# Kernel tuning notes

Hardware: AMD Instinct MI355X
Metric: run time of the kernel (lower is better)

Reference implementation:

```python
import math
import jax, jax.numpy as jnp
import numpy as np

H = 1024
N = 64
DT_MIN, DT_MAX = 0.001, 0.1
L_CONST = 4096


def setup_inputs() -> dict:
    key = jax.random.key(0)
    k1, k2 = jax.random.split(key)
    log_dt = jax.random.uniform(k1, (H,), dtype=jnp.float32) * (
        math.log(DT_MAX) - math.log(DT_MIN)
    ) + math.log(DT_MIN)
    C = jax.random.normal(k2, (H, N // 2, 2), dtype=jnp.float32)  # real view of complex C
    log_A_real = jnp.log(0.5 * jnp.ones((H, N // 2), dtype=jnp.float32))
    A_imag = math.pi * jnp.tile(jnp.arange(N // 2, dtype=jnp.float32)[None, :], (H, 1))
    return {"L": L_CONST, "log_dt": log_dt, "C": C, "log_A_real": log_A_real, "A_imag": A_imag}


def reference(L, log_dt, C, log_A_real, A_imag):
    dt = jnp.exp(log_dt)                                  # (H,)
    Cc = C[..., 0] + 1j * C[..., 1]                        # (H, N/2) complex
    A = -jnp.exp(log_A_real) + 1j * A_imag                 # (H, N/2) complex
    dtA = A * dt[:, None]                                  # (H, N/2)
    t = jnp.arange(L, dtype=jnp.float32)                   # (L,)
    exp_dtA_t = jnp.exp(dtA[:, :, None] * t)               # (H, N/2, L) complex Vandermonde
    C_eff = Cc * (jnp.exp(dtA) - 1.0) / A                  # (H, N/2)
    K = 2.0 * jnp.einsum('hn,hnl->hl', C_eff, exp_dtA_t).real  # (H, L)
    return K
```

## Files before the change

kernel.cpp:

```cpp
#include <hip/hip_runtime.h>
#include <math.h>

#define NH 32

typedef _Float16 f16;
typedef _Float16 f16x4 __attribute__((ext_vector_type(4)));
typedef float    f32x4 __attribute__((ext_vector_type(4)));

__device__ __forceinline__ float reduce2pi(float x) {
    const float INV2PI = 0.15915494309189535f;
    const float PI2_HI = 6.28125f;
    const float PI2_LO = 1.9353071795864769e-3f;
    float k = rintf(x * INV2PI);
    float r = fmaf(-k, PI2_HI, x);
    r = fmaf(-k, PI2_LO, r);
    return r;
}

__global__ __launch_bounds__(256, 4) void s4d_kernel(
    const float* __restrict__ log_dt,
    const float* __restrict__ Cv,
    const float* __restrict__ log_A_real,
    const float* __restrict__ A_imag,
    float* __restrict__ Kout,
    int L)
{
    const int h   = blockIdx.x;
    const int tid = threadIdx.x;

    __shared__ f16 Alds[32][68];
    __shared__ f16 Wlds[128][68];
    __shared__ float s_dar[NH], s_dai[NH];
    __shared__ float s_zr[NH],  s_zi[NH];
    __shared__ float s_ur[NH],  s_ui[NH];
    __shared__ float s_cer[NH], s_cei[NH];
    __shared__ float s_e1r[NH], s_e1i[NH];
    __shared__ float s_e2r[NH], s_e2i[NH];

    if (tid < NH) {
        const int n = tid;
        const float dt  = __expf(log_dt[h]);
        const float Ar  = -__expf(log_A_real[h * NH + n]);
        const float Ai  = A_imag[h * NH + n];
        const float dar = Ar * dt;
        const float dai = Ai * dt;

        float er = __expf(dar);
        float sn, cs;
        __sincosf(dai, &sn, &cs);
        float zr = er * cs, zi = er * sn;
        float edr = zr - 1.0f, edi = zi;
        float inv = 1.0f / fmaf(Ar, Ar, Ai * Ai);
        float fr  = (edr * Ar + edi * Ai) * inv;
        float fi  = (edi * Ar - edr * Ai) * inv;
        float cr  = Cv[(h * NH + n) * 2 + 0];
        float ci  = Cv[(h * NH + n) * 2 + 1];
        s_cer[n] = 2.0f * (cr * fr - ci * fi);
        s_cei[n] = 2.0f * (cr * fi + ci * fr);
        s_zr[n] = zr;  s_zi[n] = zi;

        float eu = __expf(dar * 128.0f);
        float su, cu; __sincosf(reduce2pi(dai * 128.0f), &su, &cu);
        s_ur[n] = eu * cu;  s_ui[n] = eu * su;

        float e1 = __expf(dar * 1024.0f);
        float s1, c1; __sincosf(reduce2pi(dai * 1024.0f), &s1, &c1);
        s_e1r[n] = e1 * c1;  s_e1i[n] = e1 * s1;

        float e2 = __expf(dar * 2048.0f);
        float s2, c2; __sincosf(reduce2pi(dai * 2048.0f), &s2, &c2);
        s_e2r[n] = e2 * c2;  s_e2i[n] = e2 * s2;

        s_dar[n] = dar;  s_dai[n] = dai;
    }
    __syncthreads();

    const int lane = tid & 63;
    const int wv   = tid >> 6;

    if (lane < NH) {
        const int n = lane;
        float sr, si;
        if      (wv == 0) { sr = 1.0f;      si = 0.0f; }
        else if (wv == 1) { sr = s_e1r[n];  si = s_e1i[n]; }
        else if (wv == 2) { sr = s_e2r[n];  si = s_e2i[n]; }
        else {
            sr = s_e2r[n] * s_e1r[n] - s_e2i[n] * s_e1i[n];
            si = s_e2r[n] * s_e1i[n] + s_e2i[n] * s_e1r[n];
        }
        float gr = s_cer[n] * sr - s_cei[n] * si;
        float gi = s_cer[n] * si + s_cei[n] * sr;
        const float ur = s_ur[n], ui = s_ui[n];
        #pragma unroll
        for (int s = 0; s < 8; ++s) {
            const int a = wv * 8 + s;
            Alds[a][n]      = (f16)gr;
            Alds[a][n + 32] = (f16)(-gi);
            float t = gr * ur - gi * ui;
            gi = gr * ui + gi * ur;
            gr = t;
        }
    }

    {
        const int n  = tid & 31;
        const int bg = tid >> 5;
        const float b0f = (float)(bg * 16);
        float e0 = __expf(s_dar[n] * b0f);
        float sn, cs;
        __sincosf(s_dai[n] * b0f, &sn, &cs);
        float wr = e0 * cs, wi = e0 * sn;
        const float zr = s_zr[n], zi = s_zi[n];
        #pragma unroll
        for (int i = 0; i < 16; ++i) {
            const int b = bg * 16 + i;
            Wlds[b][n]      = (f16)wr;
            Wlds[b][n + 32] = (f16)wi;
            float t = wr * zr - wi * zi;
            wi = wr * zi + wi * zr;
            wr = t;
        }
    }
    __syncthreads();

    const int r = lane & 15;
    const int q = lane >> 4;
    float* outp = Kout + (size_t)h * (size_t)L;
    #pragma unroll
    for (int mi = 0; mi < 2; ++mi) {
        #pragma unroll
        for (int ni = 0; ni < 2; ++ni) {
            f32x4 acc = {0.f, 0.f, 0.f, 0.f};
            #pragma unroll
            for (int ks = 0; ks < 4; ++ks) {
                f16x4 af = *(const f16x4*)&Alds[16 * mi + r][16 * ks + 4 * q];
                f16x4 bf = *(const f16x4*)&Wlds[32 * wv + 16 * ni + r][16 * ks + 4 * q];
                acc = __builtin_amdgcn_mfma_f32_16x16x16f16(af, bf, acc, 0, 0, 0);
            }
            const int bcol = 32 * wv + 16 * ni + r;
            #pragma unroll
            for (int reg = 0; reg < 4; ++reg) {
                const int a = 16 * mi + 4 * q + reg;
                outp[a * 128 + bcol] = acc[reg];
            }
        }
    }
}

extern "C" void kernel_launch(void* const* d_in, const int* in_sizes, int n_in,
                              void* d_out, int out_size, void* d_ws, size_t ws_size,
                              hipStream_t stream) {
    const float* log_dt     = (const float*)d_in[1];
    const float* Cv         = (const float*)d_in[2];
    const float* log_A_real = (const float*)d_in[3];
    const float* A_imag     = (const float*)d_in[4];
    float* Kout = (float*)d_out;

    const int Hn = in_sizes[1];
    const int L  = out_size / Hn;

    dim3 grid(Hn), block(256);
    hipLaunchKernelGGL(s4d_kernel, grid, block, 0, stream,
                       log_dt, Cv, log_A_real, A_imag, Kout, L);
}
```

Before: 11.32 us.

## Parallelize setup across 128 threads, interleave f16 pairs, vectorize output stores

```diff
diff --git a/kernel.cpp b/kernel.cpp
--- a/kernel.cpp
+++ b/kernel.cpp
@@ -4,6 +4,7 @@
 #define NH 32
 
 typedef _Float16 f16;
+typedef _Float16 f16x2 __attribute__((ext_vector_type(2)));
 typedef _Float16 f16x4 __attribute__((ext_vector_type(4)));
 typedef float    f32x4 __attribute__((ext_vector_type(4)));
 
@@ -37,41 +38,34 @@
     __shared__ float s_e1r[NH], s_e1i[NH];
     __shared__ float s_e2r[NH], s_e2i[NH];
 
-    if (tid < NH) {
-        const int n = tid;
+    if (tid < 128) {
+        const int n = tid & 31;
+        const int j = tid >> 5;
         const float dt  = __expf(log_dt[h]);
         const float Ar  = -__expf(log_A_real[h * NH + n]);
         const float Ai  = A_imag[h * NH + n];
         const float dar = Ar * dt;
         const float dai = Ai * dt;
-
-        float er = __expf(dar);
+        const float S = (j == 0) ? 1.0f : (j == 1) ? 128.0f
+                      : (j == 2) ? 1024.0f : 2048.0f;
+        float e = __expf(dar * S);
         float sn, cs;
-        __sincosf(dai, &sn, &cs);
-        float zr = er * cs, zi = er * sn;
-        float edr = zr - 1.0f, edi = zi;
-        float inv = 1.0f / fmaf(Ar, Ar, Ai * Ai);
-        float fr  = (edr * Ar + edi * Ai) * inv;
-        float fi  = (edi * Ar - edr * Ai) * inv;
-        float cr  = Cv[(h * NH + n) * 2 + 0];
-        float ci  = Cv[(h * NH + n) * 2 + 1];
-        s_cer[n] = 2.0f * (cr * fr - ci * fi);
-        s_cei[n] = 2.0f * (cr * fi + ci * fr);
-        s_zr[n] = zr;  s_zi[n] = zi;
-
-        float eu = __expf(dar * 128.0f);
-        float su, cu; __sincosf(reduce2pi(dai * 128.0f), &su, &cu);
-        s_ur[n] = eu * cu;  s_ui[n] = eu * su;
-
-        float e1 = __expf(dar * 1024.0f);
-        float s1, c1; __sincosf(reduce2pi(dai * 1024.0f), &s1, &c1);
-        s_e1r[n] = e1 * c1;  s_e1i[n] = e1 * s1;
-
-        float e2 = __expf(dar * 2048.0f);
-        float s2, c2; __sincosf(reduce2pi(dai * 2048.0f), &s2, &c2);
-        s_e2r[n] = e2 * c2;  s_e2i[n] = e2 * s2;
-
-        s_dar[n] = dar;  s_dai[n] = dai;
+        __sincosf(reduce2pi(dai * S), &sn, &cs);
+        float vr = e * cs, vi = e * sn;
+        if (j == 0) {
+            s_dar[n] = dar;  s_dai[n] = dai;
+            s_zr[n] = vr;    s_zi[n] = vi;
+            float edr = vr - 1.0f, edi = vi;
+            float inv = 1.0f / fmaf(Ar, Ar, Ai * Ai);
+            float fr  = (edr * Ar + edi * Ai) * inv;
+            float fi  = (edi * Ar - edr * Ai) * inv;
+            float cr  = Cv[(h * NH + n) * 2 + 0];
+            float ci  = Cv[(h * NH + n) * 2 + 1];
+            s_cer[n] = 2.0f * (cr * fr - ci * fi);
+            s_cei[n] = 2.0f * (cr * fi + ci * fr);
+        } else if (j == 1) { s_ur[n]  = vr;  s_ui[n]  = vi; }
+        else if   (j == 2) { s_e1r[n] = vr;  s_e1i[n] = vi; }
+        else               { s_e2r[n] = vr;  s_e2i[n] = vi; }
     }
     __syncthreads();
 
@@ -94,8 +88,8 @@
         #pragma unroll
         for (int s = 0; s < 8; ++s) {
             const int a = wv * 8 + s;
-            Alds[a][n]      = (f16)gr;
-            Alds[a][n + 32] = (f16)(-gi);
+            f16x2 pg = { (f16)gr, (f16)(-gi) };
+            *reinterpret_cast<f16x2*>(&Alds[a][2 * n]) = pg;
             float t = gr * ur - gi * ui;
             gi = gr * ui + gi * ur;
             gr = t;
@@ -114,8 +108,8 @@
         #pragma unroll
         for (int i = 0; i < 16; ++i) {
             const int b = bg * 16 + i;
-            Wlds[b][n]      = (f16)wr;
-            Wlds[b][n + 32] = (f16)wi;
+            f16x2 pw = { (f16)wr, (f16)wi };
+            *reinterpret_cast<f16x2*>(&Wlds[b][2 * n]) = pw;
             float t = wr * zr - wi * zi;
             wi = wr * zi + wi * zr;
             wr = t;
@@ -133,16 +127,13 @@
             f32x4 acc = {0.f, 0.f, 0.f, 0.f};
             #pragma unroll
             for (int ks = 0; ks < 4; ++ks) {
-                f16x4 af = *(const f16x4*)&Alds[16 * mi + r][16 * ks + 4 * q];
-                f16x4 bf = *(const f16x4*)&Wlds[32 * wv + 16 * ni + r][16 * ks + 4 * q];
-                acc = __builtin_amdgcn_mfma_f32_16x16x16f16(af, bf, acc, 0, 0, 0);
+                f16x4 xf = *(const f16x4*)&Wlds[32 * wv + 16 * mi + r][16 * ks + 4 * q];
+                f16x4 yf = *(const f16x4*)&Alds[16 * ni + r][16 * ks + 4 * q];
+                acc = __builtin_amdgcn_mfma_f32_16x16x16f16(xf, yf, acc, 0, 0, 0);
             }
-            const int bcol = 32 * wv + 16 * ni + r;
-            #pragma unroll
-            for (int reg = 0; reg < 4; ++reg) {
-                const int a = 16 * mi + 4 * q + reg;
-                outp[a * 128 + bcol] = acc[reg];
-            }
+            const int a  = 16 * ni + r;
+            const int b0 = 32 * wv + 16 * mi + 4 * q;
+            *(f32x4*)&outp[(size_t)a * 128 + b0] = acc;
         }
     }
 }
```

New measurement: 11.33 us. About the same (+0.1%).
